# Kernel tuning notes

Measured on AMD Instinct MI355X. Metric: run time of the kernel, lower is better.

## Reference

```python
import jax, jax.numpy as jnp
import numpy as np

N_USERS = 50000
N_ENTITIES = 150000
N_NODES = N_USERS + N_ENTITIES
N_EDGES = 3200000
BATCH = 4096
EPS = 1e-12  # F.normalize eps


def setup_inputs() -> dict:
    key = jax.random.key(0)
    ks = jax.random.split(key, 16)
    s = 0.1  # xavier-ish scale for small dims
    return {
        "user_w": jax.random.normal(ks[0], (N_USERS, 64), jnp.float32) * s,
        "entity_w": jax.random.normal(ks[1], (N_ENTITIES, 64), jnp.float32) * s,
        "W1a": jax.random.normal(ks[2], (64, 64), jnp.float32) * s,
        "b1a": jnp.zeros((64,), jnp.float32),
        "W2a": jax.random.normal(ks[3], (64, 64), jnp.float32) * s,
        "b2a": jnp.zeros((64,), jnp.float32),
        "W1b": jax.random.normal(ks[4], (64, 32), jnp.float32) * s,
        "b1b": jnp.zeros((32,), jnp.float32),
        "W2b": jax.random.normal(ks[5], (64, 32), jnp.float32) * s,
        "b2b": jnp.zeros((32,), jnp.float32),
        "values": jax.random.uniform(ks[6], (N_EDGES,), jnp.float32),
        "target": jax.random.randint(ks[7], (N_EDGES,), 0, N_NODES, jnp.int32),
        "neighbor": jax.random.randint(ks[8], (N_EDGES,), 0, N_NODES, jnp.int32),
        "user_ids": jax.random.randint(ks[9], (BATCH,), 0, N_USERS, jnp.int32),
        "pos_item_ids": jax.random.randint(ks[10], (BATCH,), 0, N_ENTITIES, jnp.int32),
        "neg_item_ids": jax.random.randint(ks[11], (BATCH,), 0, N_ENTITIES, jnp.int32),
    }


def _aggregate(features, target, neighbor, values):
    # msg = features[neighbor] * values[:, None]; h_neigh = index_add over target
    msg = features[neighbor] * values[:, None]  # (E, dim)
    return jax.ops.segment_sum(msg, target, num_segments=N_NODES)


def _gnn_layer(features, target, neighbor, values, W1, b1, W2, b2):
    h_neigh = _aggregate(features, target, neighbor, values)
    h = (features + h_neigh) @ W1 + b1 + (features * h_neigh) @ W2 + b2
    return jax.nn.leaky_relu(h, negative_slope=0.01)


def _l2norm(x):
    n = jnp.sqrt(jnp.sum(x * x, axis=1, keepdims=True))
    return x / jnp.maximum(n, EPS)


def reference(user_w, entity_w, W1a, b1a, W2a, b2a, W1b, b1b, W2b, b2b,
              values, target, neighbor, user_ids, pos_item_ids, neg_item_ids):
    all_embed = jnp.concatenate([user_w, entity_w], axis=0)  # (N, 64)
    ego = [all_embed]
    h1 = _l2norm(_gnn_layer(all_embed, target, neighbor, values, W1a, b1a, W2a, b2a))
    ego.append(h1)
    h2 = _l2norm(_gnn_layer(h1, target, neighbor, values, W1b, b1b, W2b, b2b))
    ego.append(h2)
    final_embed = jnp.concatenate(ego, axis=1)  # (N, 160)
    u = final_embed[user_ids]
    pos_i = final_embed[N_USERS + pos_item_ids]
    neg_i = final_embed[N_USERS + neg_item_ids]
    pos_scores = jnp.sum(u * pos_i, axis=1)
    neg_scores = jnp.sum(u * neg_i, axis=1)
    return (pos_scores, neg_scores)
```

## Files before the change

kernel.cpp:

```cpp
#include <hip/hip_runtime.h>

#define N_USERS    50000
#define N_ENTITIES 150000
#define N_NODES_C  200000
#define BATCH_C    4096
#define N_EDGES_C  3200000

#define CHUNK   7168
#define SG_SH   9
#define NSG     391

typedef __attribute__((ext_vector_type(2))) _Float16 h2;
typedef __attribute__((ext_vector_type(8))) _Float16 half8;
typedef __attribute__((ext_vector_type(2))) __fp16 fp16x2_s;
typedef __attribute__((ext_vector_type(4))) float float4v;


__device__ __forceinline__ h2 u2h(unsigned u) {
    union { unsigned u; h2 h; } x; x.u = u; return x.h;
}
__device__ __forceinline__ unsigned pk2h(float a, float b) {
    union { fp16x2_s h; unsigned u; } x;
    x.h = __builtin_amdgcn_cvt_pkrtz(a, b);
    return x.u;
}

__global__ __launch_bounds__(256) void tof16_k(const float* __restrict__ uw,
                                               const float* __restrict__ ew,
                                               unsigned short* __restrict__ fb)
{
    int idx = blockIdx.x * 256 + threadIdx.x;
    if (idx >= N_NODES_C * 64) return;
    const int split = N_USERS * 64;
    float x = (idx < split) ? uw[idx] : ew[idx - split];
    _Float16 hx = (_Float16)x;
    fb[idx] = *(unsigned short*)&hx;
}

__global__ __launch_bounds__(512) void zero_k(int* __restrict__ sgtot)
{
    if (threadIdx.x < NSG + 1) sgtot[threadIdx.x] = 0;
}

__global__ __launch_bounds__(256) void cnt_k(const int* __restrict__ target,
                                             int* __restrict__ sgtot, int n_edges)
{
    __shared__ int cnt[NSG];
    int c = blockIdx.x;
    int base = c * CHUNK;
    int ccount = min(CHUNK, n_edges - base);
    for (int i = threadIdx.x; i < NSG; i += 256) cnt[i] = 0;
    __syncthreads();
    for (int i = threadIdx.x; i < ccount; i += 256)
        atomicAdd(&cnt[target[base + i] >> SG_SH], 1);
    __syncthreads();
    for (int i = threadIdx.x; i < NSG; i += 256)
        if (cnt[i]) atomicAdd(&sgtot[i], cnt[i]);
}

__global__ __launch_bounds__(512) void scan_k(const int* __restrict__ sgtot,
                                              int* __restrict__ sgoff,
                                              int* __restrict__ sgcur)
{
    __shared__ int part[512];
    int t = threadIdx.x;
    int v = (t < NSG) ? sgtot[t] : 0;
    part[t] = v;
    __syncthreads();
    for (int off = 1; off < 512; off <<= 1) {
        int w = (t >= off) ? part[t - off] : 0;
        __syncthreads();
        part[t] += w;
        __syncthreads();
    }
    if (t < NSG) { sgoff[t] = part[t] - v; sgcur[t] = part[t] - v; }
    if (t == NSG - 1) sgoff[NSG] = part[t];
}

__global__ __launch_bounds__(256) void scatter_k(
    const int* __restrict__ target, const int* __restrict__ neighbor,
    const float* __restrict__ values, int* __restrict__ sgcur,
    uint2* __restrict__ tmp2, int n_edges)
{
    __shared__ uint2 buf[CHUNK];
    __shared__ int cnt[NSG], off[NSG], pos[NSG], gbase[NSG];
    int c = blockIdx.x;
    int base = c * CHUNK;
    int ccount = min(CHUNK, n_edges - base);
    for (int i = threadIdx.x; i < NSG; i += 256) { cnt[i] = 0; pos[i] = 0; }
    __syncthreads();
    for (int i = threadIdx.x; i < ccount; i += 256)
        atomicAdd(&cnt[target[base + i] >> SG_SH], 1);
    __syncthreads();
    for (int i = threadIdx.x; i < NSG; i += 256)
        if (cnt[i]) gbase[i] = atomicAdd(&sgcur[i], cnt[i]);
    if (threadIdx.x < 64) {
        int l = threadIdx.x;
        const int PER = (NSG + 63) / 64;
        int s0 = l * PER, s1 = min(s0 + PER, NSG);
        int sum = 0;
        for (int i = s0; i < s1; i++) sum += cnt[i];
        int run = sum;
        #pragma unroll
        for (int o = 1; o < 64; o <<= 1) { int v = __shfl_up(run, o); if (l >= o) run += v; }
        int excl = run - sum;
        for (int i = s0; i < s1; i++) { off[i] = excl; excl += cnt[i]; }
    }
    __syncthreads();
    for (int i = threadIdx.x; i < ccount; i += 256) {
        int t  = target[base + i];
        int sg = t >> SG_SH;
        unsigned q = (unsigned)fminf(values[base + i] * 16384.f + 0.5f, 16383.f);
        unsigned w = ((unsigned)neighbor[base + i] << 14) | q;
        int p = off[sg] + atomicAdd(&pos[sg], 1);
        buf[p] = make_uint2(w, (unsigned)t);
    }
    __syncthreads();
    for (int i = threadIdx.x; i < ccount; i += 256) {
        uint2 ed = buf[i];
        int sg = (int)(ed.y >> SG_SH);
        tmp2[(size_t)(gbase[sg] + (i - off[sg]))] = ed;
    }
}

__global__ __launch_bounds__(512) void sort2_k(
    const uint2* __restrict__ tmp2, const int* __restrict__ sgoff,
    int* __restrict__ row_ptr, unsigned* __restrict__ edges)
{
    __shared__ int cnt[512];
    __shared__ int cur[512];
    __shared__ int rp[513];
    int s = blockIdx.x;
    int node0 = s << SG_SH;
    int nn = min(512, N_NODES_C - node0);
    int sgstart = sgoff[s];
    int sgcnt = sgoff[s + 1] - sgstart;
    cnt[threadIdx.x] = 0;
    cur[threadIdx.x] = 0;
    __syncthreads();
    for (int e = threadIdx.x; e < sgcnt; e += 512)
        atomicAdd(&cnt[tmp2[(size_t)sgstart + e].y & 511u], 1);
    __syncthreads();
    if (threadIdx.x < 64) {
        int l = threadIdx.x;
        int s0 = l * 8;
        int vals[8];
        int sum = 0;
        for (int i = 0; i < 8; i++) { vals[i] = cnt[s0 + i]; sum += vals[i]; }
        int run = sum;
        #pragma unroll
        for (int o = 1; o < 64; o <<= 1) { int v = __shfl_up(run, o); if (l >= o) run += v; }
        int excl = run - sum;
        for (int i = 0; i < 8; i++) { rp[s0 + i] = excl; excl += vals[i]; }
        if (l == 63) rp[512] = excl;
    }
    __syncthreads();
    for (int i = threadIdx.x; i < nn; i += 512) row_ptr[node0 + i] = sgstart + rp[i];
    if (s == NSG - 1 && threadIdx.x == 0) row_ptr[N_NODES_C] = sgstart + sgcnt;
    for (int e = threadIdx.x; e < sgcnt; e += 512) {
        uint2 ed = tmp2[(size_t)sgstart + e];
        int tl = (int)(ed.y & 511u);
        int old = atomicAdd(&cur[tl], 1);
        edges[sgstart + rp[tl] + old] = ed.x;
    }
}

#define SPS 136
__global__ __launch_bounds__(512, 6) void layer1_pull_k(
    const unsigned short* __restrict__ fb,
    const int* __restrict__ row_ptr, const unsigned int* __restrict__ edges,
    const float* __restrict__ W1, const float* __restrict__ b1,
    const float* __restrict__ W2, const float* __restrict__ b2,
    _Float16* __restrict__ h1out, int n_nodes)
{
    __shared__ __align__(16) short wt[64 * SPS];
    __shared__ __align__(16) short sp[128 * SPS];
    __shared__ float sbias[64];

    for (int idx = threadIdx.x; idx < 64 * 64; idx += 512) {
        int kp = idx >> 6;
        int n  = idx & 63;
        int k0 = kp * 2, k1 = k0 + 1;
        float w0 = (k0 < 64) ? W1[k0 * 64 + n] : W2[(k0 - 64) * 64 + n];
        float w1 = (k1 < 64) ? W1[k1 * 64 + n] : W2[(k1 - 64) * 64 + n];
        *(unsigned*)&wt[n * SPS + k0] = pk2h(w0, w1);
    }
    if (threadIdx.x < 64) sbias[threadIdx.x] = b1[threadIdx.x] + b2[threadIdx.x];
    __syncthreads();

    int wv   = threadIdx.x >> 6;
    int lane = threadIdx.x & 63;
    int g    = lane >> 4;
    int q    = lane & 15;
    const uint2* fb2 = (const uint2*)fb;

    int nb0 = blockIdx.x * 128;
    const float QS = 1.f / 16384.f;

    for (int i = 0; i < 16; i += 4) {
        int mA = wv * 16 + i;
        int nodeBase = nb0 + mA;

        int es0 = 0, ee0 = 0, es1 = 0, ee1 = 0, es2 = 0, ee2 = 0, es3 = 0, ee3 = 0;
        if (nodeBase     < n_nodes) { es0 = row_ptr[nodeBase];     ee0 = row_ptr[nodeBase + 1]; }
        if (nodeBase + 1 < n_nodes) { es1 = row_ptr[nodeBase + 1]; ee1 = row_ptr[nodeBase + 2]; }
        if (nodeBase + 2 < n_nodes) { es2 = row_ptr[nodeBase + 2]; ee2 = row_ptr[nodeBase + 3]; }
        if (nodeBase + 3 < n_nodes) { es3 = row_ptr[nodeBase + 3]; ee3 = row_ptr[nodeBase + 4]; }

        h2 aLo0 = (h2){0, 0}, aHi0 = (h2){0, 0};
        h2 aLo1 = (h2){0, 0}, aHi1 = (h2){0, 0};
        h2 aLo2 = (h2){0, 0}, aHi2 = (h2){0, 0};
        h2 aLo3 = (h2){0, 0}, aHi3 = (h2){0, 0};

        int b0 = es0, b1c = es1, b2c = es2, b3c = es3;
        while (b0 < ee0 || b1c < ee1 || b2c < ee2 || b3c < ee3) {
            int c0 = ee0 - b0;  c0 = c0 < 0 ? 0 : (c0 > 64 ? 64 : c0);
            int c1 = ee1 - b1c; c1 = c1 < 0 ? 0 : (c1 > 64 ? 64 : c1);
            int c2 = ee2 - b2c; c2 = c2 < 0 ? 0 : (c2 > 64 ? 64 : c2);
            int c3 = ee3 - b3c; c3 = c3 < 0 ? 0 : (c3 > 64 ? 64 : c3);
            unsigned ev0 = (lane < c0) ? edges[b0 + lane]  : 0u;
            unsigned ev1 = (lane < c1) ? edges[b1c + lane] : 0u;
            unsigned ev2 = (lane < c2) ? edges[b2c + lane] : 0u;
            unsigned ev3 = (lane < c3) ? edges[b3c + lane] : 0u;
            int jm0 = (c0 + 3) >> 2;
            int jm1 = (c1 + 3) >> 2;
            int jm2 = (c2 + 3) >> 2;
            int jm3 = (c3 + 3) >> 2;
            int jm = max(max(jm0, jm1), max(jm2, jm3));
            #pragma unroll 4
            for (int j = 0; j < jm; j++) {
                unsigned w0 = (unsigned)__shfl((int)ev0, j * 4 + g);
                unsigned w1 = (unsigned)__shfl((int)ev1, j * 4 + g);
                unsigned w2 = (unsigned)__shfl((int)ev2, j * 4 + g);
                unsigned w3 = (unsigned)__shfl((int)ev3, j * 4 + g);
                uint2 d0 = fb2[(size_t)(w0 >> 14) * 16 + q];
                uint2 d1 = fb2[(size_t)(w1 >> 14) * 16 + q];
                uint2 d2 = fb2[(size_t)(w2 >> 14) * 16 + q];
                uint2 d3 = fb2[(size_t)(w3 >> 14) * 16 + q];
                _Float16 v0 = (_Float16)((float)(w0 & 16383u) * QS);
                _Float16 v1 = (_Float16)((float)(w1 & 16383u) * QS);
                _Float16 v2 = (_Float16)((float)(w2 & 16383u) * QS);
                _Float16 v3 = (_Float16)((float)(w3 & 16383u) * QS);
                h2 vv0 = (h2){v0, v0};
                h2 vv1 = (h2){v1, v1};
                h2 vv2 = (h2){v2, v2};
                h2 vv3 = (h2){v3, v3};
                aLo0 += u2h(d0.x) * vv0;  aHi0 += u2h(d0.y) * vv0;
                aLo1 += u2h(d1.x) * vv1;  aHi1 += u2h(d1.y) * vv1;
                aLo2 += u2h(d2.x) * vv2;  aHi2 += u2h(d2.y) * vv2;
                aLo3 += u2h(d3.x) * vv3;  aHi3 += u2h(d3.y) * vv3;
            }
            b0 += 64; b1c += 64; b2c += 64; b3c += 64;
        }

        float ac[4][4];
        ac[0][0] = (float)aLo0.x; ac[0][1] = (float)aLo0.y; ac[0][2] = (float)aHi0.x; ac[0][3] = (float)aHi0.y;
        ac[1][0] = (float)aLo1.x; ac[1][1] = (float)aLo1.y; ac[1][2] = (float)aHi1.x; ac[1][3] = (float)aHi1.y;
        ac[2][0] = (float)aLo2.x; ac[2][1] = (float)aLo2.y; ac[2][2] = (float)aHi2.x; ac[2][3] = (float)aHi2.y;
        ac[3][0] = (float)aLo3.x; ac[3][1] = (float)aLo3.y; ac[3][2] = (float)aHi3.x; ac[3][3] = (float)aHi3.y;
        #pragma unroll
        for (int s = 0; s < 4; s++)
            #pragma unroll
            for (int c = 0; c < 4; c++) {
                ac[s][c] += __shfl_xor(ac[s][c], 16);
                ac[s][c] += __shfl_xor(ac[s][c], 32);
            }

        int hseg = g >> 1;
        int prod = g & 1;
        int r0 = mA + (hseg << 1);
        int r1 = r0 + 1;
        int nd0 = nb0 + r0, nd1 = nb0 + r1;
        uint2 d0 = make_uint2(0u, 0u), d1 = make_uint2(0u, 0u);
        if (nd0 < n_nodes) d0 = fb2[(size_t)nd0 * 16 + q];
        if (nd1 < n_nodes) d1 = fb2[(size_t)nd1 * 16 + q];
        float a00 = hseg ? ac[2][0] : ac[0][0];
        float a01 = hseg ? ac[2][1] : ac[0][1];
        float a02 = hseg ? ac[2][2] : ac[0][2];
        float a03 = hseg ? ac[2][3] : ac[0][3];
        float a10 = hseg ? ac[3][0] : ac[1][0];
        float a11 = hseg ? ac[3][1] : ac[1][1];
        float a12 = hseg ? ac[3][2] : ac[1][2];
        float a13 = hseg ? ac[3][3] : ac[1][3];
        h2 s0l = u2h(d0.x), s0h = u2h(d0.y);
        h2 s1l = u2h(d1.x), s1h = u2h(d1.y);
        float f00 = (float)s0l.x, f01 = (float)s0l.y, f02 = (float)s0h.x, f03 = (float)s0h.y;
        float f10 = (float)s1l.x, f11 = (float)s1l.y, f12 = (float)s1h.x, f13 = (float)s1h.y;
        float x00 = prod ? f00 * a00 : f00 + a00;
        float x01 = prod ? f01 * a01 : f01 + a01;
        float x02 = prod ? f02 * a02 : f02 + a02;
        float x03 = prod ? f03 * a03 : f03 + a03;
        float x10 = prod ? f10 * a10 : f10 + a10;
        float x11 = prod ? f11 * a11 : f11 + a11;
        float x12 = prod ? f12 * a12 : f12 + a12;
        float x13 = prod ? f13 * a13 : f13 + a13;
        uint2 pk;
        pk.x = pk2h(x00, x01);
        pk.y = pk2h(x02, x03);
        *(uint2*)&sp[r0 * SPS + prod * 64 + q * 4] = pk;
        pk.x = pk2h(x10, x11);
        pk.y = pk2h(x12, x13);
        *(uint2*)&sp[r1 * SPS + prod * 64 + q * 4] = pk;
    }

    __builtin_amdgcn_wave_barrier();
    asm volatile("s_waitcnt lgkmcnt(0)" ::: "memory");
    __builtin_amdgcn_wave_barrier();

    float4v c0, c1, c2, c3;
    {
        float bv0 = sbias[q];
        float bv1 = sbias[16 + q];
        float bv2 = sbias[32 + q];
        float bv3 = sbias[48 + q];
        c0 = (float4v){bv0, bv0, bv0, bv0};
        c1 = (float4v){bv1, bv1, bv1, bv1};
        c2 = (float4v){bv2, bv2, bv2, bv2};
        c3 = (float4v){bv3, bv3, bv3, bv3};
    }
    #pragma unroll
    for (int kk = 0; kk < 4; kk++) {
        int ko = kk * 32 + g * 8;
        half8 a   = *(const half8*)&sp[(wv * 16 + q) * SPS + ko];
        half8 bb0 = *(const half8*)&wt[(q)      * SPS + ko];
        half8 bb1 = *(const half8*)&wt[(16 + q) * SPS + ko];
        half8 bb2 = *(const half8*)&wt[(32 + q) * SPS + ko];
        half8 bb3 = *(const half8*)&wt[(48 + q) * SPS + ko];
        c0 = __builtin_amdgcn_mfma_f32_16x16x32_f16(a, bb0, c0, 0, 0, 0);
        c1 = __builtin_amdgcn_mfma_f32_16x16x32_f16(a, bb1, c1, 0, 0, 0);
        c2 = __builtin_amdgcn_mfma_f32_16x16x32_f16(a, bb2, c2, 0, 0, 0);
        c3 = __builtin_amdgcn_mfma_f32_16x16x32_f16(a, bb3, c3, 0, 0, 0);
    }

    float ss[4];
    #pragma unroll
    for (int r = 0; r < 4; r++) {
        c0[r] = (c0[r] > 0.f) ? c0[r] : 0.01f * c0[r];
        c1[r] = (c1[r] > 0.f) ? c1[r] : 0.01f * c1[r];
        c2[r] = (c2[r] > 0.f) ? c2[r] : 0.01f * c2[r];
        c3[r] = (c3[r] > 0.f) ? c3[r] : 0.01f * c3[r];
        ss[r] = c0[r]*c0[r] + c1[r]*c1[r] + c2[r]*c2[r] + c3[r]*c3[r];
        #pragma unroll
        for (int mm = 1; mm < 16; mm <<= 1) ss[r] += __shfl_xor(ss[r], mm);
        ss[r] = 1.f / fmaxf(sqrtf(ss[r]), 1e-12f);
    }
    #pragma unroll
    for (int r = 0; r < 4; r++) {
        int node_r = nb0 + wv * 16 + g * 4 + r;
        if (node_r >= n_nodes) continue;
        size_t row = (size_t)node_r * 64;
        h1out[row +      q] = (_Float16)(c0[r] * ss[r]);
        h1out[row + 16 + q] = (_Float16)(c1[r] * ss[r]);
        h1out[row + 32 + q] = (_Float16)(c2[r] * ss[r]);
        h1out[row + 48 + q] = (_Float16)(c3[r] * ss[r]);
    }
}

__device__ __forceinline__ float layer2_row(
    const _Float16* __restrict__ h1,
    const int* __restrict__ row_ptr, const unsigned int* __restrict__ edges,
    const float* sW1, const float* sW2, const float* sb,
    int node, int lane)
{
    int es = row_ptr[node];
    int ee = row_ptr[node + 1];
    const float QS = 1.f / 16384.f;
    float g = 0.f;
    for (int base = es; base < ee; base += 64) {
        int cnt = min(64, ee - base);
        unsigned ev = (lane < cnt) ? edges[base + lane] : 0u;
        int j = 0;
        for (; j + 4 <= cnt; j += 4) {
            unsigned e0 = (unsigned)__shfl((int)ev, j);
            unsigned e1 = (unsigned)__shfl((int)ev, j + 1);
            unsigned e2 = (unsigned)__shfl((int)ev, j + 2);
            unsigned e3 = (unsigned)__shfl((int)ev, j + 3);
            float f0 = (float)h1[(size_t)(e0 >> 14) * 64 + lane];
            float f1 = (float)h1[(size_t)(e1 >> 14) * 64 + lane];
            float f2 = (float)h1[(size_t)(e2 >> 14) * 64 + lane];
            float f3 = (float)h1[(size_t)(e3 >> 14) * 64 + lane];
            g += (float)(e0 & 16383u) * QS * f0 + (float)(e1 & 16383u) * QS * f1
               + (float)(e2 & 16383u) * QS * f2 + (float)(e3 & 16383u) * QS * f3;
        }
        for (; j < cnt; j++) {
            unsigned e0 = (unsigned)__shfl((int)ev, j);
            float f0 = (float)h1[(size_t)(e0 >> 14) * 64 + lane];
            g += (float)(e0 & 16383u) * QS * f0;
        }
    }
    float f = (float)h1[(size_t)node * 64 + lane];
    float s = f + g;
    float p = f * g;
    int j = lane & 31;
    float acc = sb[j];
    #pragma unroll
    for (int k = 0; k < 64; k++) {
        float sk = __shfl(s, k);
        float pk = __shfl(p, k);
        acc += sk * sW1[k * 32 + j] + pk * sW2[k * 32 + j];
    }
    acc = (acc > 0.f) ? acc : 0.01f * acc;
    float sq = acc * acc;
    #pragma unroll
    for (int m = 1; m < 32; m <<= 1) sq += __shfl_xor(sq, m);
    return acc / fmaxf(sqrtf(sq), 1e-12f);
}

__global__ __launch_bounds__(256) void score_k(
    const float* __restrict__ uw, const float* __restrict__ ew,
    const _Float16* __restrict__ h1,
    const int* __restrict__ row_ptr, const unsigned int* __restrict__ edges,
    const float* __restrict__ W1b, const float* __restrict__ b1b,
    const float* __restrict__ W2b, const float* __restrict__ b2b,
    const int* __restrict__ uid, const int* __restrict__ pid,
    const int* __restrict__ nid, float* __restrict__ out)
{
    __shared__ float sW1[64 * 32];
    __shared__ float sW2[64 * 32];
    __shared__ float sb[32];
    for (int i = threadIdx.x; i < 64 * 32; i += 256) { sW1[i] = W1b[i]; sW2[i] = W2b[i]; }
    if (threadIdx.x < 32) sb[threadIdx.x] = b1b[threadIdx.x] + b2b[threadIdx.x];
    __syncthreads();

    int wave = threadIdx.x >> 6;
    int lane = threadIdx.x & 63;
    int i = blockIdx.x * 4 + wave;
    if (i >= BATCH_C) return;

    int un = uid[i];
    int pe = pid[i];
    int ne = nid[i];
    int pn = N_USERS + pe;
    int nn = N_USERS + ne;

    float acc01p, acc01n;
    {
        float u  = uw[(size_t)un * 64 + lane];
        float pv = ew[(size_t)pe * 64 + lane];
        float nv = ew[(size_t)ne * 64 + lane];
        acc01p = u * pv;
        acc01n = u * nv;
        float u1 = (float)h1[(size_t)un * 64 + lane];
        acc01p += u1 * (float)h1[(size_t)pn * 64 + lane];
        acc01n += u1 * (float)h1[(size_t)nn * 64 + lane];
    }

    float h2u = layer2_row(h1, row_ptr, edges, sW1, sW2, sb, un, lane);
    float h2p = layer2_row(h1, row_ptr, edges, sW1, sW2, sb, pn, lane);
    float h2n = layer2_row(h1, row_ptr, edges, sW1, sW2, sb, nn, lane);
    float p2 = h2u * h2p;
    float n2 = h2u * h2n;
    #pragma unroll
    for (int m = 1; m < 32; m <<= 1) { p2 += __shfl_xor(p2, m); n2 += __shfl_xor(n2, m); }

    #pragma unroll
    for (int m = 1; m < 64; m <<= 1) { acc01p += __shfl_xor(acc01p, m); acc01n += __shfl_xor(acc01n, m); }

    if (lane == 0) {
        out[i]           = acc01p + p2;
        out[BATCH_C + i] = acc01n + n2;
    }
}

extern "C" void kernel_launch(void* const* d_in, const int* in_sizes, int n_in,
                              void* d_out, int out_size, void* d_ws, size_t ws_size,
                              hipStream_t stream) {
    const float* uw   = (const float*)d_in[0];
    const float* ew   = (const float*)d_in[1];
    const float* W1a  = (const float*)d_in[2];
    const float* b1a  = (const float*)d_in[3];
    const float* W2a  = (const float*)d_in[4];
    const float* b2a  = (const float*)d_in[5];
    const float* W1b  = (const float*)d_in[6];
    const float* b1b  = (const float*)d_in[7];
    const float* W2b  = (const float*)d_in[8];
    const float* b2b  = (const float*)d_in[9];
    const float* values   = (const float*)d_in[10];
    const int*   target   = (const int*)d_in[11];
    const int*   neighbor = (const int*)d_in[12];
    const int*   uid  = (const int*)d_in[13];
    const int*   pid  = (const int*)d_in[14];
    const int*   nid  = (const int*)d_in[15];

    const int n_edges = in_sizes[10];

    char* ws = (char*)d_ws;
    int*  row_ptr    = (int*)ws;   ws += 801792;
    int*  sgtot      = (int*)ws;   ws += 4096;
    int*  sgoff      = (int*)ws;   ws += 4096;
    int*  sgcur      = (int*)ws;   ws += 4096;
    unsigned int*   edges = (unsigned int*)ws;   ws += (size_t)N_EDGES_C * 4;
    unsigned short* fb    = (unsigned short*)ws; ws += (size_t)N_NODES_C * 64 * 2;
    uint2*          tmp2  = (uint2*)ws;
    _Float16*       h1    = (_Float16*)ws;

    const int layer_blocks = (N_NODES_C + 127) / 128;
    const int conv_blocks  = (N_NODES_C * 64 + 255) / 256;
    const int nchunks      = (n_edges + CHUNK - 1) / CHUNK;

    tof16_k<<<conv_blocks, 256, 0, stream>>>(uw, ew, fb);

    zero_k<<<1, 512, 0, stream>>>(sgtot);
    cnt_k<<<nchunks, 256, 0, stream>>>(target, sgtot, n_edges);
    scan_k<<<1, 512, 0, stream>>>(sgtot, sgoff, sgcur);
    scatter_k<<<nchunks, 256, 0, stream>>>(target, neighbor, values, sgcur, tmp2, n_edges);
    sort2_k<<<NSG, 512, 0, stream>>>(tmp2, sgoff, row_ptr, edges);

    layer1_pull_k<<<layer_blocks, 512, 0, stream>>>(fb, row_ptr, edges,
                                                    W1a, b1a, W2a, b2a, h1, N_NODES_C);

    score_k<<<BATCH_C / 4, 256, 0, stream>>>(uw, ew, h1, row_ptr, edges,
                                             W1b, b1b, W2b, b2b,
                                             uid, pid, nid, (float*)d_out);
}
```

Before: 359.3 us.

## Replace two-level bucket sort CSR build with global-atomic counting sort

Builds the CSR adjacency with a per-node global atomic histogram, a block-sum scan to form row_ptr, and a direct atomic placement pass. This replaces the supergroup bucket scatter and in-shared-memory second sort. It removes the 8-byte temporary edge buffer and one full pass over the edges. In exchange it relies on millions of global atomics to random L2 addresses and scattered uncoalesced writes, and edge order within a row becomes nondeterministic.

```diff
diff --git a/kernel.cpp b/kernel.cpp
--- a/kernel.cpp
+++ b/kernel.cpp
@@ -6,9 +6,7 @@
 #define BATCH_C    4096
 #define N_EDGES_C  3200000
 
-#define CHUNK   7168
-#define SG_SH   9
-#define NSG     391
+#define NB 391
 
 typedef __attribute__((ext_vector_type(2))) _Float16 h2;
 typedef __attribute__((ext_vector_type(8))) _Float16 half8;
@@ -37,34 +35,46 @@
     fb[idx] = *(unsigned short*)&hx;
 }
 
-__global__ __launch_bounds__(512) void zero_k(int* __restrict__ sgtot)
-{
-    if (threadIdx.x < NSG + 1) sgtot[threadIdx.x] = 0;
-}
-
-__global__ __launch_bounds__(256) void cnt_k(const int* __restrict__ target,
-                                             int* __restrict__ sgtot, int n_edges)
-{
-    __shared__ int cnt[NSG];
-    int c = blockIdx.x;
-    int base = c * CHUNK;
-    int ccount = min(CHUNK, n_edges - base);
-    for (int i = threadIdx.x; i < NSG; i += 256) cnt[i] = 0;
-    __syncthreads();
-    for (int i = threadIdx.x; i < ccount; i += 256)
-        atomicAdd(&cnt[target[base + i] >> SG_SH], 1);
-    __syncthreads();
-    for (int i = threadIdx.x; i < NSG; i += 256)
-        if (cnt[i]) atomicAdd(&sgtot[i], cnt[i]);
-}
-
-__global__ __launch_bounds__(512) void scan_k(const int* __restrict__ sgtot,
-                                              int* __restrict__ sgoff,
-                                              int* __restrict__ sgcur)
+__global__ __launch_bounds__(512) void zero_k(int* __restrict__ ncnt)
+{
+    int i = blockIdx.x * 512 + threadIdx.x;
+    if (i < N_NODES_C) ncnt[i] = 0;
+}
+
+__global__ __launch_bounds__(256) void hist_k(const int* __restrict__ target,
+                                              int* __restrict__ ncnt, int n_edges)
+{
+    int i = blockIdx.x * 256 + threadIdx.x;
+    int stride = gridDim.x * 256;
+    for (; i < n_edges; i += stride)
+        atomicAdd(&ncnt[target[i]], 1);
+}
+
+__global__ __launch_bounds__(512) void bsum_k(const int* __restrict__ ncnt,
+                                              int* __restrict__ bsum)
+{
+    __shared__ int ws[8];
+    int node = blockIdx.x * 512 + threadIdx.x;
+    int v = (node < N_NODES_C) ? ncnt[node] : 0;
+    #pragma unroll
+    for (int m = 1; m < 64; m <<= 1) v += __shfl_xor(v, m);
+    if ((threadIdx.x & 63) == 0) ws[threadIdx.x >> 6] = v;
+    __syncthreads();
+    if (threadIdx.x == 0) {
+        int s = 0;
+        #pragma unroll
+        for (int i = 0; i < 8; i++) s += ws[i];
+        bsum[blockIdx.x] = s;
+    }
+}
+
+__global__ __launch_bounds__(512) void bscan_k(const int* __restrict__ bsum,
+                                               int* __restrict__ boff,
+                                               int* __restrict__ row_ptr)
 {
     __shared__ int part[512];
     int t = threadIdx.x;
-    int v = (t < NSG) ? sgtot[t] : 0;
+    int v = (t < NB) ? bsum[t] : 0;
     part[t] = v;
     __syncthreads();
     for (int off = 1; off < 512; off <<= 1) {
@@ -73,95 +83,58 @@
         part[t] += w;
         __syncthreads();
     }
-    if (t < NSG) { sgoff[t] = part[t] - v; sgcur[t] = part[t] - v; }
-    if (t == NSG - 1) sgoff[NSG] = part[t];
-}
-
-__global__ __launch_bounds__(256) void scatter_k(
-    const int* __restrict__ target, const int* __restrict__ neighbor,
-    const float* __restrict__ values, int* __restrict__ sgcur,
-    uint2* __restrict__ tmp2, int n_edges)
-{
-    __shared__ uint2 buf[CHUNK];
-    __shared__ int cnt[NSG], off[NSG], pos[NSG], gbase[NSG];
-    int c = blockIdx.x;
-    int base = c * CHUNK;
-    int ccount = min(CHUNK, n_edges - base);
-    for (int i = threadIdx.x; i < NSG; i += 256) { cnt[i] = 0; pos[i] = 0; }
-    __syncthreads();
-    for (int i = threadIdx.x; i < ccount; i += 256)
-        atomicAdd(&cnt[target[base + i] >> SG_SH], 1);
-    __syncthreads();
-    for (int i = threadIdx.x; i < NSG; i += 256)
-        if (cnt[i]) gbase[i] = atomicAdd(&sgcur[i], cnt[i]);
-    if (threadIdx.x < 64) {
-        int l = threadIdx.x;
-        const int PER = (NSG + 63) / 64;
-        int s0 = l * PER, s1 = min(s0 + PER, NSG);
-        int sum = 0;
-        for (int i = s0; i < s1; i++) sum += cnt[i];
-        int run = sum;
-        #pragma unroll
-        for (int o = 1; o < 64; o <<= 1) { int v = __shfl_up(run, o); if (l >= o) run += v; }
-        int excl = run - sum;
-        for (int i = s0; i < s1; i++) { off[i] = excl; excl += cnt[i]; }
-    }
-    __syncthreads();
-    for (int i = threadIdx.x; i < ccount; i += 256) {
-        int t  = target[base + i];
-        int sg = t >> SG_SH;
-        unsigned q = (unsigned)fminf(values[base + i] * 16384.f + 0.5f, 16383.f);
-        unsigned w = ((unsigned)neighbor[base + i] << 14) | q;
-        int p = off[sg] + atomicAdd(&pos[sg], 1);
-        buf[p] = make_uint2(w, (unsigned)t);
-    }
-    __syncthreads();
-    for (int i = threadIdx.x; i < ccount; i += 256) {
-        uint2 ed = buf[i];
-        int sg = (int)(ed.y >> SG_SH);
-        tmp2[(size_t)(gbase[sg] + (i - off[sg]))] = ed;
-    }
-}
-
-__global__ __launch_bounds__(512) void sort2_k(
-    const uint2* __restrict__ tmp2, const int* __restrict__ sgoff,
-    int* __restrict__ row_ptr, unsigned* __restrict__ edges)
-{
-    __shared__ int cnt[512];
-    __shared__ int cur[512];
-    __shared__ int rp[513];
-    int s = blockIdx.x;
-    int node0 = s << SG_SH;
-    int nn = min(512, N_NODES_C - node0);
-    int sgstart = sgoff[s];
-    int sgcnt = sgoff[s + 1] - sgstart;
-    cnt[threadIdx.x] = 0;
-    cur[threadIdx.x] = 0;
-    __syncthreads();
-    for (int e = threadIdx.x; e < sgcnt; e += 512)
-        atomicAdd(&cnt[tmp2[(size_t)sgstart + e].y & 511u], 1);
+    if (t < NB) boff[t] = part[t] - v;
+    if (t == NB - 1) { boff[NB] = part[t]; row_ptr[N_NODES_C] = part[t]; }
+}
+
+__global__ __launch_bounds__(512) void rowptr_k(const int* __restrict__ ncnt,
+                                                const int* __restrict__ boff,
+                                                int* __restrict__ row_ptr,
+                                                int* __restrict__ nodecur)
+{
+    __shared__ int c[512];
+    __shared__ int rp[512];
+    int b = blockIdx.x;
+    int node = b * 512 + threadIdx.x;
+    int v = (node < N_NODES_C) ? ncnt[node] : 0;
+    c[threadIdx.x] = v;
     __syncthreads();
     if (threadIdx.x < 64) {
         int l = threadIdx.x;
         int s0 = l * 8;
         int vals[8];
         int sum = 0;
-        for (int i = 0; i < 8; i++) { vals[i] = cnt[s0 + i]; sum += vals[i]; }
+        #pragma unroll
+        for (int i = 0; i < 8; i++) { vals[i] = c[s0 + i]; sum += vals[i]; }
         int run = sum;
         #pragma unroll
-        for (int o = 1; o < 64; o <<= 1) { int v = __shfl_up(run, o); if (l >= o) run += v; }
+        for (int o = 1; o < 64; o <<= 1) { int w = __shfl_up(run, o); if (l >= o) run += w; }
         int excl = run - sum;
+        #pragma unroll
         for (int i = 0; i < 8; i++) { rp[s0 + i] = excl; excl += vals[i]; }
-        if (l == 63) rp[512] = excl;
-    }
-    __syncthreads();
-    for (int i = threadIdx.x; i < nn; i += 512) row_ptr[node0 + i] = sgstart + rp[i];
-    if (s == NSG - 1 && threadIdx.x == 0) row_ptr[N_NODES_C] = sgstart + sgcnt;
-    for (int e = threadIdx.x; e < sgcnt; e += 512) {
-        uint2 ed = tmp2[(size_t)sgstart + e];
-        int tl = (int)(ed.y & 511u);
-        int old = atomicAdd(&cur[tl], 1);
-        edges[sgstart + rp[tl] + old] = ed.x;
+    }
+    __syncthreads();
+    if (node < N_NODES_C) {
+        int s = boff[b] + rp[threadIdx.x];
+        row_ptr[node] = s;
+        nodecur[node] = s;
+    }
+}
+
+__global__ __launch_bounds__(256) void place_k(const int* __restrict__ target,
+                                               const int* __restrict__ neighbor,
+                                               const float* __restrict__ values,
+                                               int* __restrict__ nodecur,
+                                               unsigned* __restrict__ edges, int n_edges)
+{
+    int i = blockIdx.x * 256 + threadIdx.x;
+    int stride = gridDim.x * 256;
+    for (; i < n_edges; i += stride) {
+        int t = target[i];
+        unsigned q = (unsigned)fminf(values[i] * 16384.f + 0.5f, 16383.f);
+        unsigned w = ((unsigned)neighbor[i] << 14) | q;
+        int pos = atomicAdd(&nodecur[t], 1);
+        edges[pos] = w;
     }
 }
 
@@ -486,25 +459,26 @@
 
     char* ws = (char*)d_ws;
     int*  row_ptr    = (int*)ws;   ws += 801792;
-    int*  sgtot      = (int*)ws;   ws += 4096;
-    int*  sgoff      = (int*)ws;   ws += 4096;
-    int*  sgcur      = (int*)ws;   ws += 4096;
+    int*  ncnt       = (int*)ws;   ws += 800768;
+    int*  nodecur    = (int*)ws;   ws += 800768;
+    int*  bsum       = (int*)ws;   ws += 2048;
+    int*  boff       = (int*)ws;   ws += 2048;
     unsigned int*   edges = (unsigned int*)ws;   ws += (size_t)N_EDGES_C * 4;
     unsigned short* fb    = (unsigned short*)ws; ws += (size_t)N_NODES_C * 64 * 2;
-    uint2*          tmp2  = (uint2*)ws;
     _Float16*       h1    = (_Float16*)ws;
 
     const int layer_blocks = (N_NODES_C + 127) / 128;
     const int conv_blocks  = (N_NODES_C * 64 + 255) / 256;
-    const int nchunks      = (n_edges + CHUNK - 1) / CHUNK;
+    const int edge_blocks  = 2048;
 
     tof16_k<<<conv_blocks, 256, 0, stream>>>(uw, ew, fb);
 
-    zero_k<<<1, 512, 0, stream>>>(sgtot);
-    cnt_k<<<nchunks, 256, 0, stream>>>(target, sgtot, n_edges);
-    scan_k<<<1, 512, 0, stream>>>(sgtot, sgoff, sgcur);
-    scatter_k<<<nchunks, 256, 0, stream>>>(target, neighbor, values, sgcur, tmp2, n_edges);
-    sort2_k<<<NSG, 512, 0, stream>>>(tmp2, sgoff, row_ptr, edges);
+    zero_k<<<NB, 512, 0, stream>>>(ncnt);
+    hist_k<<<edge_blocks, 256, 0, stream>>>(target, ncnt, n_edges);
+    bsum_k<<<NB, 512, 0, stream>>>(ncnt, bsum);
+    bscan_k<<<1, 512, 0, stream>>>(bsum, boff, row_ptr);
+    rowptr_k<<<NB, 512, 0, stream>>>(ncnt, boff, row_ptr, nodecur);
+    place_k<<<edge_blocks, 256, 0, stream>>>(target, neighbor, values, nodecur, edges, n_edges);
 
     layer1_pull_k<<<layer_blocks, 512, 0, stream>>>(fb, row_ptr, edges,
                                                     W1a, b1a, W2a, b2a, h1, N_NODES_C);
```

Result: slower. 605.8 us (+68.6%).
